# Optimization experiments

Hardware: AMD Instinct MI355X
Metric: run time of the kernel (lower is better)

Reference implementation:

```python
import jax, jax.numpy as jnp
import numpy as np

B, N, E = 4, 10000, 80000
DN, DE, DG = 64, 16, 32
D, H, L = 256, 8, 3
DH = D // H


def _ln(x, s, b, eps=1e-6):
    m = x.mean(-1, keepdims=True)
    v = ((x - m) ** 2).mean(-1, keepdims=True)
    return (x - m) * jax.lax.rsqrt(v + eps) * s + b


def setup_inputs() -> dict:
    key = jax.random.key(0)
    ks = jax.random.split(key, 20)
    sc = 0.02
    p = {}
    # graph data
    p['node_features'] = jax.random.normal(ks[0], (B, N, DN), jnp.float32)
    p['edge_features'] = jax.random.normal(ks[1], (B, E, DE), jnp.float32)
    p['global_features'] = jax.random.normal(ks[2], (B, 1, DG), jnp.float32)
    p['edge_list'] = jax.random.randint(ks[3], (B, E, 2), 0, N)
    p['edge_mask'] = jax.random.bernoulli(ks[4], 0.9, (B, E))
    p['node_mask'] = jax.random.bernoulli(ks[5], 0.95, (B, N))
    p['current_agent_node_ind'] = jax.random.randint(ks[6], (B,), 0, N)
    # input projections
    p['W_node_in'] = jax.random.normal(ks[7], (DN + DG, D)) * sc
    p['b_node_in'] = jnp.zeros((D,))
    p['W_edge_in'] = jax.random.normal(ks[8], (DE, D)) * sc
    p['b_edge_in'] = jnp.zeros((D,))
    p['ln_edge_s'] = jnp.ones((D,)); p['ln_edge_b'] = jnp.zeros((D,))
    # stacked GCN layers: message Dense over concat([h_sender, edge_feat])
    p['gcn_W'] = jax.random.normal(ks[9], (L, 2 * D, D)) * sc
    p['gcn_b'] = jnp.zeros((L, D))
    p['ln_s'] = jnp.ones((L, D)); p['ln_b'] = jnp.zeros((L, D))
    # PGAT params
    p['lnq_s'] = jnp.ones((D,)); p['lnq_b'] = jnp.zeros((D,))
    p['lnk_s'] = jnp.ones((D,)); p['lnk_b'] = jnp.zeros((D,))
    p['Wq'] = jax.random.normal(ks[10], (D, D)) * sc; p['bq'] = jnp.zeros((D,))
    p['Wk'] = jax.random.normal(ks[11], (D, D)) * sc; p['bk'] = jnp.zeros((D,))
    p['Wv'] = jax.random.normal(ks[12], (D, D)) * sc; p['bv'] = jnp.zeros((D,))
    p['Wo'] = jax.random.normal(ks[13], (D, D)) * sc; p['bo'] = jnp.zeros((D,))
    p['lnf_s'] = jnp.ones((D,)); p['lnf_b'] = jnp.zeros((D,))
    return p


def reference(node_features, edge_features, global_features, edge_list, edge_mask,
              node_mask, current_agent_node_ind,
              W_node_in, b_node_in, W_edge_in, b_edge_in, ln_edge_s, ln_edge_b,
              gcn_W, gcn_b, ln_s, ln_b,
              lnq_s, lnq_b, lnk_s, lnk_b, Wq, bq, Wk, bk, Wv, bv, Wo, bo,
              lnf_s, lnf_b):
    senders = edge_list[..., 0]
    receivers = edge_list[..., 1]
    # masked-edge handling: original sets indices to -1 so scatter drops them;
    # we mask explicitly (same math) with safe indices.
    s_safe = jnp.where(edge_mask, senders, 0)
    r_safe = jnp.where(edge_mask, receivers, 0)
    emf = edge_mask.astype(node_features.dtype)  # [B, E]

    gf = jnp.broadcast_to(global_features, node_features.shape[:-1] + (DG,))
    h = jnp.concatenate([node_features, gf], axis=-1) @ W_node_in + b_node_in  # [B,N,D]
    e = jax.nn.relu(_ln(edge_features @ W_edge_in + b_edge_in, ln_edge_s, ln_edge_b))  # [B,E,D]

    seg = jax.vmap(lambda m, r: jax.ops.segment_sum(m, r, num_segments=N))
    deg = jnp.maximum(seg(emf[..., None], r_safe), 1.0)  # [B,N,1]

    for i in range(L):
        hn = jax.nn.relu(_ln(h, ln_s[i], ln_b[i]))
        hs = jnp.take_along_axis(hn, s_safe[..., None], axis=-2)  # [B,E,D] gather
        msg = jnp.concatenate([hs, e], axis=-1) @ gcn_W[i] + gcn_b[i]
        msg = msg * emf[..., None]
        agg = seg(msg, r_safe) / deg  # normalized (mean) aggregation
        h = hn + agg  # residual

    # agent node gather: [B,1,D]
    q_in = jnp.take_along_axis(h, current_agent_node_ind[:, None, None], axis=-2)

    # PGAT: masked multi-head attention of agent query over all nodes
    q = _ln(q_in, lnq_s, lnq_b)
    k = _ln(h, lnk_s, lnk_b)
    Q = (q @ Wq + bq).reshape(B, 1, H, DH)
    K = (k @ Wk + bk).reshape(B, N, H, DH)
    V = (k @ Wv + bv).reshape(B, N, H, DH)
    scores = jnp.einsum('bqhd,bkhd->bhqk', Q, K) / jnp.asarray(np.sqrt(DH), Q.dtype)
    scores = jnp.where(node_mask[:, None, None, :], scores, -1e9)
    attn = jax.nn.softmax(scores, axis=-1)
    o = jnp.einsum('bhqk,bkhd->bqhd', attn, V).reshape(B, 1, D)
    x = q_in + (o @ Wo + bo)  # residual
    x = jax.nn.relu(_ln(x, lnf_s, lnf_b))
    return x.reshape(B, D)  # rearrange '... n d -> ... (n d)' with n=1
```

## Files before the change

kernel.cpp:

```cpp
#include <hip/hip_runtime.h>
#include <hip/hip_bf16.h>

#define B_ 4
#define N_ 10000
#define E_ 80000
#define D_ 256
#define BN_ (B_*N_)
#define MPAD 40064

typedef __attribute__((ext_vector_type(8))) short short8;
typedef __attribute__((ext_vector_type(4))) float f32x4;
typedef __attribute__((ext_vector_type(4))) unsigned short u16x4;

static __device__ __forceinline__ float wave_sum(float v){
  #pragma unroll
  for(int o=32;o>0;o>>=1) v += __shfl_xor(v, o);
  return v;
}

static __device__ __forceinline__ float block_sum(float v, float* red){
  v = wave_sum(v);
  int w = threadIdx.x >> 6;
  if((threadIdx.x & 63) == 0) red[w] = v;
  __syncthreads();
  float r = (red[0] + red[1]) + (red[2] + red[3]);
  __syncthreads();
  return r;
}

static __device__ __forceinline__ unsigned short f2bf(float f){
  unsigned u = __float_as_uint(f);
  return (unsigned short)((u + 0x7fffu + ((u>>16)&1u)) >> 16);
}
static __device__ __forceinline__ float bf2f(unsigned short b){
  return __uint_as_float(((unsigned)b) << 16);
}

__global__ __launch_bounds__(256) void k_node_in(
    const float* __restrict__ nf, const float* __restrict__ gf,
    const float* __restrict__ W, const float* __restrict__ bias,
    const float* __restrict__ lns, const float* __restrict__ lnb,
    unsigned short* __restrict__ hnbf){
  __shared__ float in_s[16][96];
  __shared__ float h_s[16][256];
  int base = blockIdx.x * 16;
  int tid = threadIdx.x;
  for(int idx = tid; idx < 16*96; idx += 256){
    int i = idx / 96, k = idx - i*96;
    int row = base + i;
    int b = row / N_;
    float v = (k < 64) ? nf[(size_t)row*64 + k] : gf[b*32 + (k-64)];
    in_s[i][k] = v;
  }
  __syncthreads();
  int c = tid;
  float acc[16];
  #pragma unroll
  for(int i=0;i<16;i++) acc[i]=0.f;
  for(int k=0;k<96;k+=4){
    float w0 = W[(k+0)*D_+c], w1 = W[(k+1)*D_+c];
    float w2 = W[(k+2)*D_+c], w3 = W[(k+3)*D_+c];
    #pragma unroll
    for(int i=0;i<16;i++){
      float4 a = *reinterpret_cast<const float4*>(&in_s[i][k]);
      acc[i] += a.x*w0 + a.y*w1 + a.z*w2 + a.w*w3;
    }
  }
  float bc = bias[c];
  #pragma unroll
  for(int i=0;i<16;i++) h_s[i][c] = acc[i] + bc;
  __syncthreads();
  int wv = tid>>6, lane = tid&63;
  float4 s4 = *reinterpret_cast<const float4*>(&lns[lane*4]);
  float4 b4 = *reinterpret_cast<const float4*>(&lnb[lane*4]);
  #pragma unroll
  for(int rr=0; rr<4; ++rr){
    int i = wv*4 + rr;
    float4 x = *reinterpret_cast<const float4*>(&h_s[i][lane*4]);
    float sum = x.x+x.y+x.z+x.w;
    float sq = x.x*x.x+x.y*x.y+x.z*x.z+x.w*x.w;
    #pragma unroll
    for(int o=32;o>0;o>>=1){ sum += __shfl_xor(sum,o); sq += __shfl_xor(sq,o); }
    float mean = sum*(1.f/256.f);
    float var = sq*(1.f/256.f) - mean*mean;
    float rs = rsqrtf(var + 1e-6f);
    u16x4 o;
    o.x = f2bf(fmaxf((x.x-mean)*rs*s4.x + b4.x, 0.f));
    o.y = f2bf(fmaxf((x.y-mean)*rs*s4.y + b4.y, 0.f));
    o.z = f2bf(fmaxf((x.z-mean)*rs*s4.z + b4.z, 0.f));
    o.w = f2bf(fmaxf((x.w-mean)*rs*s4.w + b4.w, 0.f));
    *reinterpret_cast<u16x4*>(&hnbf[(size_t)(base+i)*D_ + lane*4]) = o;
  }
}

__global__ __launch_bounds__(256) void k_hist(
    const int* __restrict__ el, const int* __restrict__ emask,
    int* __restrict__ counts){
  int e = blockIdx.x*256 + threadIdx.x;
  if(e >= B_*E_) return;
  if(emask[e]){
    int b = e / E_;
    int r = el[(size_t)e*2 + 1];
    atomicAdd(&counts[b*N_ + r], 1);
  }
}

__global__ __launch_bounds__(1024) void k_scan(
    const int* __restrict__ counts, int* __restrict__ offsets){
  __shared__ int wsum[16];
  int tid = threadIdx.x;
  int base = tid*40;
  int s = 0;
  #pragma unroll
  for(int i=0;i<40;i++){ int idx=base+i; s += (idx<BN_)?counts[idx]:0; }
  int lane = tid&63, w = tid>>6;
  int incl = s;
  #pragma unroll
  for(int o=1;o<64;o<<=1){ int v=__shfl_up(incl,o); if(lane>=o) incl+=v; }
  if(lane==63) wsum[w]=incl;
  __syncthreads();
  if(tid<16){
    int v = wsum[tid];
    #pragma unroll
    for(int o=1;o<16;o<<=1){ int u=__shfl_up(v,o); if(tid>=o) v+=u; }
    wsum[tid]=v;
  }
  __syncthreads();
  int run = ((w>0)?wsum[w-1]:0) + incl - s;
  #pragma unroll
  for(int i=0;i<40;i++){
    int idx=base+i;
    if(idx<BN_){ offsets[idx]=run; run += counts[idx]; }
  }
  if(tid==1023) offsets[BN_]=run;
}

__global__ __launch_bounds__(256) void k_eprep(
    const float* __restrict__ W, const float* __restrict__ be,
    float* __restrict__ prep){
  int t = threadIdx.x;
  int i = t >> 4, j = t & 15;
  float m = 0.f;
  for(int c=0;c<256;c++) m += W[i*256+c]*W[j*256+c];
  prep[t] = m;
  if(t < 16){
    float v=0.f, wb=0.f;
    for(int c=0;c<256;c++){ v += W[t*256+c]*be[c]; wb += W[t*256+c]; }
    prep[256+t] = v;
    prep[272+t] = wb*(1.f/256.f);
  }
  if(t == 0){
    float bb=0.f, ss=0.f;
    for(int c=0;c<256;c++){ bb += be[c]; ss += be[c]*be[c]; }
    prep[288] = bb*(1.f/256.f);
    prep[289] = ss;
  }
}

__global__ __launch_bounds__(256) void k_fill(
    const int* __restrict__ el, const int* __restrict__ emask,
    const float* __restrict__ ef, const float* __restrict__ prep,
    const int* __restrict__ offsets, int* __restrict__ cursor,
    int* __restrict__ s_send, float* __restrict__ ef_slot,
    float* __restrict__ stats){
  __shared__ float M_s[290];
  for(int i=threadIdx.x; i<290; i+=256) M_s[i] = prep[i];
  __syncthreads();
  int e = blockIdx.x*256 + threadIdx.x;
  if(e >= B_*E_) return;
  if(!emask[e]) return;
  int b = e / E_;
  int s = el[(size_t)e*2], r = el[(size_t)e*2 + 1];
  int bn = b*N_ + r;
  int pos = offsets[bn] + atomicAdd(&cursor[bn], 1);
  s_send[pos] = b*N_ + s;
  const float4* src = reinterpret_cast<const float4*>(ef + (size_t)e*16);
  float4 f0=src[0], f1=src[1], f2=src[2], f3=src[3];
  float4* dst = reinterpret_cast<float4*>(ef_slot + (size_t)pos*16);
  dst[0]=f0; dst[1]=f1; dst[2]=f2; dst[3]=f3;
  float f[16] = {f0.x,f0.y,f0.z,f0.w, f1.x,f1.y,f1.z,f1.w,
                 f2.x,f2.y,f2.z,f2.w, f3.x,f3.y,f3.z,f3.w};
  float mean = M_s[288];
  #pragma unroll
  for(int k=0;k<16;k++) mean += f[k]*M_s[272+k];
  float q = M_s[289];
  #pragma unroll
  for(int i=0;i<16;i++){
    float pi = 2.f*M_s[256+i];
    #pragma unroll
    for(int j=0;j<16;j++) pi += M_s[i*16+j]*f[j];
    q += f[i]*pi;
  }
  float var = q*(1.f/256.f) - mean*mean;
  float rstd = rsqrtf(var + 1e-6f);
  stats[(size_t)pos*2]   = mean;
  stats[(size_t)pos*2+1] = rstd;
}

__global__ __launch_bounds__(256) void k_wt(
    const float* __restrict__ gcnW, unsigned short* __restrict__ Wt){
  __shared__ float sm[32][33];
  int bid = blockIdx.x;
  int l = bid >> 7;
  int t = bid & 127;
  int k0 = (t >> 3)*32, n0 = (t & 7)*32;
  int r = threadIdx.x >> 3;
  int c4 = (threadIdx.x & 7)*4;
  const float* src = gcnW + (size_t)l*512*256;
  float4 v = *reinterpret_cast<const float4*>(&src[(size_t)(k0+r)*256 + n0 + c4]);
  sm[r][c4+0]=v.x; sm[r][c4+1]=v.y; sm[r][c4+2]=v.z; sm[r][c4+3]=v.w;
  __syncthreads();
  u16x4 o;
  o.x = f2bf(sm[c4+0][r]); o.y = f2bf(sm[c4+1][r]);
  o.z = f2bf(sm[c4+2][r]); o.w = f2bf(sm[c4+3][r]);
  *reinterpret_cast<u16x4*>(&Wt[(size_t)l*256*512 + (size_t)(n0+r)*512 + k0 + c4]) = o;
}

#define PROJ(F0,F1,F2,F3,COMP) (be4.COMP \
  + F0.x*w[0].COMP + F0.y*w[1].COMP + F0.z*w[2].COMP + F0.w*w[3].COMP \
  + F1.x*w[4].COMP + F1.y*w[5].COMP + F1.z*w[6].COMP + F1.w*w[7].COMP \
  + F2.x*w[8].COMP + F2.y*w[9].COMP + F2.z*w[10].COMP + F2.w*w[11].COMP \
  + F3.x*w[12].COMP + F3.y*w[13].COMP + F3.z*w[14].COMP + F3.w*w[15].COMP)

__global__ __launch_bounds__(256) void k_se_wave(
    const float* __restrict__ ef_slot, const float* __restrict__ stats,
    const float* __restrict__ W, const float* __restrict__ be,
    const float* __restrict__ lns, const float* __restrict__ lnb,
    const int* __restrict__ offsets, unsigned short* __restrict__ Abf){
  int bn = blockIdx.x*4 + (threadIdx.x>>6);
  int lane = threadIdx.x & 63;
  int c = lane*4;
  float4 w[16];
  #pragma unroll
  for(int k=0;k<16;k++) w[k] = *reinterpret_cast<const float4*>(&W[k*D_ + c]);
  float4 be4 = *reinterpret_cast<const float4*>(&be[c]);
  float4 s4  = *reinterpret_cast<const float4*>(&lns[c]);
  float4 b4  = *reinterpret_cast<const float4*>(&lnb[c]);
  int beg = __builtin_amdgcn_readfirstlane(offsets[bn]);
  int end = __builtin_amdgcn_readfirstlane(offsets[bn+1]);
  float a0=0.f,a1=0.f,a2=0.f,a3=0.f;
  int slot = beg;
  for(; slot+2 <= end; slot += 2){
    const float4* e0 = reinterpret_cast<const float4*>(ef_slot + (size_t)slot*16);
    const float4* e1 = reinterpret_cast<const float4*>(ef_slot + (size_t)(slot+1)*16);
    float2 st0 = *reinterpret_cast<const float2*>(stats + (size_t)slot*2);
    float2 st1 = *reinterpret_cast<const float2*>(stats + (size_t)(slot+1)*2);
    float4 f0=e0[0], f1=e0[1], f2=e0[2], f3=e0[3];
    float4 g0=e1[0], g1=e1[1], g2=e1[2], g3=e1[3];
    float t0=PROJ(f0,f1,f2,f3,x), t1=PROJ(f0,f1,f2,f3,y);
    float t2=PROJ(f0,f1,f2,f3,z), t3=PROJ(f0,f1,f2,f3,w);
    float u0=PROJ(g0,g1,g2,g3,x), u1=PROJ(g0,g1,g2,g3,y);
    float u2=PROJ(g0,g1,g2,g3,z), u3=PROJ(g0,g1,g2,g3,w);
    float m0=st0.x, r0=st0.y, m1=st1.x, r1=st1.y;
    a0 += fmaxf((t0-m0)*r0*s4.x + b4.x, 0.f) + fmaxf((u0-m1)*r1*s4.x + b4.x, 0.f);
    a1 += fmaxf((t1-m0)*r0*s4.y + b4.y, 0.f) + fmaxf((u1-m1)*r1*s4.y + b4.y, 0.f);
    a2 += fmaxf((t2-m0)*r0*s4.z + b4.z, 0.f) + fmaxf((u2-m1)*r1*s4.z + b4.z, 0.f);
    a3 += fmaxf((t3-m0)*r0*s4.w + b4.w, 0.f) + fmaxf((u3-m1)*r1*s4.w + b4.w, 0.f);
  }
  if(slot < end){
    const float4* e0 = reinterpret_cast<const float4*>(ef_slot + (size_t)slot*16);
    float2 st0 = *reinterpret_cast<const float2*>(stats + (size_t)slot*2);
    float4 f0=e0[0], f1=e0[1], f2=e0[2], f3=e0[3];
    float t0=PROJ(f0,f1,f2,f3,x), t1=PROJ(f0,f1,f2,f3,y);
    float t2=PROJ(f0,f1,f2,f3,z), t3=PROJ(f0,f1,f2,f3,w);
    float m0=st0.x, r0=st0.y;
    a0 += fmaxf((t0-m0)*r0*s4.x + b4.x, 0.f);
    a1 += fmaxf((t1-m0)*r0*s4.y + b4.y, 0.f);
    a2 += fmaxf((t2-m0)*r0*s4.z + b4.z, 0.f);
    a3 += fmaxf((t3-m0)*r0*s4.w + b4.w, 0.f);
  }
  u16x4 o; o.x=f2bf(a0); o.y=f2bf(a1); o.z=f2bf(a2); o.w=f2bf(a3);
  *reinterpret_cast<u16x4*>(Abf + (size_t)bn*512 + 256 + c) = o;
}

__global__ __launch_bounds__(256) void k_ln_relu(
    const float* __restrict__ h, const float* __restrict__ s,
    const float* __restrict__ b, unsigned short* __restrict__ hnbf){
  int row = blockIdx.x*4 + (threadIdx.x>>6);
  int lane = threadIdx.x & 63;
  int c = lane*4;
  float4 x = *reinterpret_cast<const float4*>(&h[(size_t)row*D_ + c]);
  float sum = x.x+x.y+x.z+x.w;
  float sq = x.x*x.x+x.y*x.y+x.z*x.z+x.w*x.w;
  #pragma unroll
  for(int o=32;o>0;o>>=1){ sum += __shfl_xor(sum,o); sq += __shfl_xor(sq,o); }
  float mean = sum*(1.f/256.f);
  float var = sq*(1.f/256.f) - mean*mean;
  float rs = rsqrtf(var + 1e-6f);
  float4 s4 = *reinterpret_cast<const float4*>(&s[c]);
  float4 b4 = *reinterpret_cast<const float4*>(&b[c]);
  u16x4 o;
  o.x = f2bf(fmaxf((x.x-mean)*rs*s4.x + b4.x, 0.f));
  o.y = f2bf(fmaxf((x.y-mean)*rs*s4.y + b4.y, 0.f));
  o.z = f2bf(fmaxf((x.z-mean)*rs*s4.z + b4.z, 0.f));
  o.w = f2bf(fmaxf((x.w-mean)*rs*s4.w + b4.w, 0.f));
  *reinterpret_cast<u16x4*>(&hnbf[(size_t)row*D_ + c]) = o;
}

__global__ __launch_bounds__(256) void k_agg(
    const unsigned short* __restrict__ hnbf, const int* __restrict__ offsets,
    const int* __restrict__ s_send, unsigned short* __restrict__ Abf){
  int bn = blockIdx.x*4 + (threadIdx.x>>6);
  int lane = threadIdx.x & 63;
  int beg = __builtin_amdgcn_readfirstlane(offsets[bn]);
  int end = __builtin_amdgcn_readfirstlane(offsets[bn+1]);
  float a0=0.f,a1=0.f,a2=0.f,a3=0.f;
  int slot = beg;
  for(; slot+4 <= end; slot += 4){
    int sr0 = s_send[slot],   sr1 = s_send[slot+1];
    int sr2 = s_send[slot+2], sr3 = s_send[slot+3];
    u16x4 v0 = *reinterpret_cast<const u16x4*>(hnbf + (size_t)sr0*D_ + lane*4);
    u16x4 v1 = *reinterpret_cast<const u16x4*>(hnbf + (size_t)sr1*D_ + lane*4);
    u16x4 v2 = *reinterpret_cast<const u16x4*>(hnbf + (size_t)sr2*D_ + lane*4);
    u16x4 v3 = *reinterpret_cast<const u16x4*>(hnbf + (size_t)sr3*D_ + lane*4);
    a0 += bf2f(v0.x)+bf2f(v1.x)+bf2f(v2.x)+bf2f(v3.x);
    a1 += bf2f(v0.y)+bf2f(v1.y)+bf2f(v2.y)+bf2f(v3.y);
    a2 += bf2f(v0.z)+bf2f(v1.z)+bf2f(v2.z)+bf2f(v3.z);
    a3 += bf2f(v0.w)+bf2f(v1.w)+bf2f(v2.w)+bf2f(v3.w);
  }
  for(; slot < end; ++slot){
    int sr = s_send[slot];
    u16x4 v = *reinterpret_cast<const u16x4*>(hnbf + (size_t)sr*D_ + lane*4);
    a0 += bf2f(v.x); a1 += bf2f(v.y); a2 += bf2f(v.z); a3 += bf2f(v.w);
  }
  u16x4 o; o.x=f2bf(a0); o.y=f2bf(a1); o.z=f2bf(a2); o.w=f2bf(a3);
  *reinterpret_cast<u16x4*>(Abf + (size_t)bn*512 + lane*4) = o;
}

__global__ __launch_bounds__(256) void k_gemm_mfma(
    const unsigned short* __restrict__ Abf,
    const unsigned short* __restrict__ Wt,
    const float* __restrict__ bias,
    const int* __restrict__ counts,
    const unsigned short* __restrict__ hnbf,
    float* __restrict__ hout){
  __shared__ unsigned short A_s[128*32];
  __shared__ unsigned short B_s[128*32];
  int bid = blockIdx.x;
  int row0 = (bid>>1)*128;
  int col0 = (bid&1)*128;
  int tid = threadIdx.x;
  int lane = tid & 63;
  int wid = tid >> 6;
  int wr = wid >> 1, wc = wid & 1;
  f32x4 acc[4][4];
  #pragma unroll
  for(int m=0;m<4;m++)
    #pragma unroll
    for(int n=0;n<4;n++) acc[m][n] = (f32x4){0.f,0.f,0.f,0.f};

  int sr = tid >> 1;
  int sc0 = (tid & 1)*2;
  const unsigned short* agp = Abf + (size_t)(row0+sr)*512;
  const unsigned short* bgp = Wt  + (size_t)(col0+sr)*512;
  unsigned swA0 = (unsigned)(sr*64 + (((sc0  ) ^ (sr&3))*16));
  unsigned swA1 = (unsigned)(sr*64 + (((sc0+1) ^ (sr&3))*16));
  int frow = lane & 15;
  int fsw = (lane >> 4) ^ (lane & 3);

  for(int k0=0; k0<512; k0+=32){
    short8 a0 = *reinterpret_cast<const short8*>(agp + k0 + sc0*8);
    short8 a1 = *reinterpret_cast<const short8*>(agp + k0 + sc0*8 + 8);
    short8 b0 = *reinterpret_cast<const short8*>(bgp + k0 + sc0*8);
    short8 b1 = *reinterpret_cast<const short8*>(bgp + k0 + sc0*8 + 8);
    __syncthreads();
    *reinterpret_cast<short8*>((char*)A_s + swA0) = a0;
    *reinterpret_cast<short8*>((char*)A_s + swA1) = a1;
    *reinterpret_cast<short8*>((char*)B_s + swA0) = b0;
    *reinterpret_cast<short8*>((char*)B_s + swA1) = b1;
    __syncthreads();
    short8 af[4], bfr[4];
    #pragma unroll
    for(int m=0;m<4;m++){
      int r = wr*64 + m*16 + frow;
      af[m] = *reinterpret_cast<const short8*>((const char*)A_s + r*64 + fsw*16);
    }
    #pragma unroll
    for(int n=0;n<4;n++){
      int r = wc*64 + n*16 + frow;
      bfr[n] = *reinterpret_cast<const short8*>((const char*)B_s + r*64 + fsw*16);
    }
    #pragma unroll
    for(int m=0;m<4;m++)
      #pragma unroll
      for(int n=0;n<4;n++)
        acc[m][n] = __builtin_amdgcn_mfma_f32_16x16x32_bf16(af[m], bfr[n], acc[m][n], 0, 0, 0);
  }
  #pragma unroll
  for(int m=0;m<4;m++){
    #pragma unroll
    for(int n=0;n<4;n++){
      int col = col0 + wc*64 + n*16 + (lane&15);
      int rbase = row0 + wr*64 + m*16 + (lane>>4)*4;
      float bcol = bias[col];
      #pragma unroll
      for(int j=0;j<4;j++){
        int r = rbase + j;
        if(r < BN_){
          float cnt = (float)counts[r];
          float inv = 1.f / fmaxf(cnt, 1.f);
          hout[(size_t)r*D_ + col] = bf2f(hnbf[(size_t)r*D_ + col]) + (acc[m][n][j] + cnt*bcol)*inv;
        }
      }
    }
  }
}

__global__ __launch_bounds__(256) void k_qprep(
    const float* __restrict__ h, const int* __restrict__ agent,
    const float* __restrict__ lnq_s, const float* __restrict__ lnq_b,
    const float* __restrict__ Wq, const float* __restrict__ bq,
    const float* __restrict__ Wk, const float* __restrict__ bk,
    float* __restrict__ q_in, float* __restrict__ Wq_eff,
    float* __restrict__ qconst){
  __shared__ float q_s[256];
  __shared__ float Q_s[256];
  __shared__ float red[4];
  int b = blockIdx.x, c = threadIdx.x;
  size_t row = (size_t)(b*N_ + agent[b]);
  float x = h[row*D_ + c];
  q_in[b*D_ + c] = x;
  float s1 = block_sum(x, red);
  float mean = s1*(1.f/256.f);
  float d = x - mean;
  float s2 = block_sum(d*d, red);
  float q = d * rsqrtf(s2*(1.f/256.f) + 1e-6f) * lnq_s[c] + lnq_b[c];
  q_s[c] = q;
  __syncthreads();
  float acc = bq[c];
  for(int k=0;k<256;k++) acc += q_s[k]*Wq[k*D_ + c];
  Q_s[c] = acc;
  __syncthreads();
  const float scale = 0.17677669529663687f;
  for(int idx=c; idx<2048; idx+=256){
    int hh = idx >> 8, dd = idx & 255;
    const float4* wk4 = reinterpret_cast<const float4*>(&Wk[(size_t)dd*D_ + hh*32]);
    const float4* q4  = reinterpret_cast<const float4*>(&Q_s[hh*32]);
    float t = 0.f;
    #pragma unroll
    for(int k4=0;k4<8;k4++){
      float4 w = wk4[k4]; float4 qq = q4[k4];
      t += w.x*qq.x + w.y*qq.y + w.z*qq.z + w.w*qq.w;
    }
    Wq_eff[b*2048 + hh*256 + dd] = t*scale;
  }
  if(c < 8){
    float t = 0.f;
    for(int dh=0; dh<32; dh++) t += Q_s[c*32+dh]*bk[c*32+dh];
    qconst[b*8 + c] = t*scale;
  }
}

__global__ __launch_bounds__(256) void k_scores(
    const float* __restrict__ h, const float* __restrict__ lnk_s,
    const float* __restrict__ lnk_b, const float* __restrict__ Wq_eff,
    const float* __restrict__ qconst, const int* __restrict__ nmask,
    unsigned short* __restrict__ kbuf, float* __restrict__ scores){
  __shared__ float wq_s[2048];
  int row0 = blockIdx.x * 4;
  int b = row0 / N_;
  for(int i=threadIdx.x; i<2048; i+=256) wq_s[i] = Wq_eff[b*2048 + i];
  __syncthreads();
  int wave = threadIdx.x >> 6, lane = threadIdx.x & 63;
  int row = row0 + wave;
  int n = row - b*N_;
  int c = lane*4;
  float4 x = *reinterpret_cast<const float4*>(&h[(size_t)row*D_ + c]);
  float sum = x.x+x.y+x.z+x.w;
  float sq = x.x*x.x+x.y*x.y+x.z*x.z+x.w*x.w;
  #pragma unroll
  for(int o=32;o>0;o>>=1){ sum += __shfl_xor(sum,o); sq += __shfl_xor(sq,o); }
  float mean = sum*(1.f/256.f);
  float var = sq*(1.f/256.f) - mean*mean;
  float rs = rsqrtf(var + 1e-6f);
  float4 s4 = *reinterpret_cast<const float4*>(&lnk_s[c]);
  float4 b4 = *reinterpret_cast<const float4*>(&lnk_b[c]);
  float4 kv;
  kv.x = (x.x-mean)*rs*s4.x + b4.x;
  kv.y = (x.y-mean)*rs*s4.y + b4.y;
  kv.z = (x.z-mean)*rs*s4.z + b4.z;
  kv.w = (x.w-mean)*rs*s4.w + b4.w;
  u16x4 kb; kb.x=f2bf(kv.x); kb.y=f2bf(kv.y); kb.z=f2bf(kv.z); kb.w=f2bf(kv.w);
  *reinterpret_cast<u16x4*>(&kbuf[(size_t)row*D_ + c]) = kb;
  bool valid = nmask[row] != 0;
  #pragma unroll
  for(int hh=0; hh<8; hh++){
    float4 w = *reinterpret_cast<const float4*>(&wq_s[hh*256 + c]);
    float p = kv.x*w.x + kv.y*w.y + kv.z*w.z + kv.w*w.w;
    p = wave_sum(p);
    if(lane==0) scores[(size_t)(b*8+hh)*N_ + n] = valid ? (p + qconst[b*8+hh]) : -1e9f;
  }
}

__global__ __launch_bounds__(256) void k_softA(
    const float* __restrict__ scores, float* __restrict__ pm,
    float* __restrict__ ps){
  __shared__ float red[4];
  int bh = blockIdx.x / 10;
  int c0 = (blockIdx.x % 10) * 1000;
  int tid = threadIdx.x;
  float m = -3e38f;
  for(int n=tid; n<1000; n+=256) m = fmaxf(m, scores[(size_t)bh*N_ + c0 + n]);
  #pragma unroll
  for(int o=32;o>0;o>>=1) m = fmaxf(m, __shfl_xor(m,o));
  if((tid&63)==0) red[tid>>6] = m;
  __syncthreads();
  m = fmaxf(fmaxf(red[0],red[1]), fmaxf(red[2],red[3]));
  __syncthreads();
  float s = 0.f;
  for(int n=tid; n<1000; n+=256) s += __expf(scores[(size_t)bh*N_ + c0 + n] - m);
  s = block_sum(s, red);
  if(tid==0){ pm[blockIdx.x] = m; ps[blockIdx.x] = s; }
}

__global__ __launch_bounds__(64) void k_softB(
    const float* __restrict__ pm, const float* __restrict__ ps,
    float* __restrict__ mg, float* __restrict__ inv){
  int t = threadIdx.x;
  if(t < 32){
    float m = -3e38f;
    #pragma unroll
    for(int c=0;c<10;c++) m = fmaxf(m, pm[t*10+c]);
    float s = 0.f;
    #pragma unroll
    for(int c=0;c<10;c++) s += ps[t*10+c]*__expf(pm[t*10+c]-m);
    mg[t] = m;
    inv[t] = 1.f/s;
  }
}

__global__ __launch_bounds__(256) void k_kbar(
    const unsigned short* __restrict__ kbuf, const float* __restrict__ scores,
    const float* __restrict__ mg, const float* __restrict__ inv,
    float* __restrict__ kbar){
  __shared__ float p_s[8][40];
  int b = blockIdx.x / 250;
  int n0 = (blockIdx.x % 250) * 40;
  for(int i=threadIdx.x; i<8*40; i+=256){
    int hh = i/40, nn = i - hh*40;
    p_s[hh][nn] = __expf(scores[(size_t)(b*8+hh)*N_ + n0 + nn] - mg[b*8+hh]);
  }
  __syncthreads();
  int c = threadIdx.x;
  float acc[8] = {0.f,0.f,0.f,0.f,0.f,0.f,0.f,0.f};
  for(int nn=0; nn<40; ++nn){
    float kv = bf2f(kbuf[(size_t)(b*N_ + n0 + nn)*D_ + c]);
    #pragma unroll
    for(int hh=0;hh<8;hh++) acc[hh] += p_s[hh][nn]*kv;
  }
  #pragma unroll
  for(int hh=0;hh<8;hh++)
    atomicAdd(&kbar[(b*8+hh)*D_ + c], acc[hh]*inv[b*8+hh]);
}

__global__ __launch_bounds__(256) void k_final(
    const float* __restrict__ kbar, const float* __restrict__ Wv,
    const float* __restrict__ bv, const float* __restrict__ Wo,
    const float* __restrict__ bo, const float* __restrict__ q_in,
    const float* __restrict__ lnf_s, const float* __restrict__ lnf_b,
    float* __restrict__ out){
  __shared__ float kb_s[2048];
  __shared__ float o_s[256];
  __shared__ float red[4];
  int b = blockIdx.x, c = threadIdx.x;
  for(int i=c; i<2048; i+=256) kb_s[i] = kbar[b*2048 + i];
  __syncthreads();
  int hh = c >> 5;
  float o = bv[c];
  for(int d=0; d<256; d++) o += kb_s[hh*256 + d]*Wv[(size_t)d*D_ + c];
  o_s[c] = o;
  __syncthreads();
  float y = bo[c] + q_in[b*D_ + c];
  for(int d=0; d<256; d++) y += o_s[d]*Wo[(size_t)d*D_ + c];
  float s1 = block_sum(y, red);
  float mean = s1*(1.f/256.f);
  float dd = y - mean;
  float s2 = block_sum(dd*dd, red);
  float v = dd * rsqrtf(s2*(1.f/256.f) + 1e-6f) * lnf_s[c] + lnf_b[c];
  out[b*D_ + c] = fmaxf(v, 0.f);
}

extern "C" void kernel_launch(void* const* d_in, const int* in_sizes, int n_in,
                              void* d_out, int out_size, void* d_ws, size_t ws_size,
                              hipStream_t stream){
  const float* nf    = (const float*)d_in[0];
  const float* ef    = (const float*)d_in[1];
  const float* gf    = (const float*)d_in[2];
  const int*   el    = (const int*)d_in[3];
  const int*   emask = (const int*)d_in[4];
  const int*   nmask = (const int*)d_in[5];
  const int*   agent = (const int*)d_in[6];
  const float* W_node = (const float*)d_in[7];
  const float* b_node = (const float*)d_in[8];
  const float* W_edge = (const float*)d_in[9];
  const float* b_edge = (const float*)d_in[10];
  const float* ln_e_s = (const float*)d_in[11];
  const float* ln_e_b = (const float*)d_in[12];
  const float* gcn_W  = (const float*)d_in[13];
  const float* gcn_b  = (const float*)d_in[14];
  const float* ln_s   = (const float*)d_in[15];
  const float* ln_b   = (const float*)d_in[16];
  const float* lnq_s  = (const float*)d_in[17];
  const float* lnq_b  = (const float*)d_in[18];
  const float* lnk_s  = (const float*)d_in[19];
  const float* lnk_b  = (const float*)d_in[20];
  const float* Wq = (const float*)d_in[21];
  const float* bq = (const float*)d_in[22];
  const float* Wv = (const float*)d_in[25];
  const float* bv = (const float*)d_in[26];
  const float* Wk = (const float*)d_in[23];
  const float* bk = (const float*)d_in[24];
  const float* Wo = (const float*)d_in[27];
  const float* bo = (const float*)d_in[28];
  const float* lnf_s = (const float*)d_in[29];
  const float* lnf_b = (const float*)d_in[30];
  float* out = (float*)d_out;

  const size_t ND = (size_t)BN_*D_;
  char* w = (char*)d_ws;
  float* h_buf = (float*)w;                   w += ND*4;
  unsigned short* hn_bf = (unsigned short*)w; w += (size_t)MPAD*D_*2;
  unsigned short* A_bf = (unsigned short*)w;  w += (size_t)MPAD*512*2;
  unsigned short* Wt = (unsigned short*)w;    w += (size_t)3*256*512*2;
  float* scores = (float*)w;                  w += (size_t)B_*8*N_*4;
  float* q_in = (float*)w;                    w += B_*D_*4;
  float* Wq_eff = (float*)w;                  w += B_*8*D_*4;
  float* qconst = (float*)w;                  w += B_*8*4;
  float* pm = (float*)w;                      w += 320*4;
  float* ps = (float*)w;                      w += 320*4;
  float* mg = (float*)w;                      w += 32*4;
  float* invs = (float*)w;                    w += 32*4;
  float* kbar = (float*)w;                    w += B_*8*D_*4;
  float* prep = (float*)w;                    w += 512*4;
  int* counts = (int*)w;                      w += BN_*4;
  int* cursor = (int*)w;                      w += BN_*4;
  int* offsets = (int*)w;                     w += (BN_+1)*4;
  int* s_send = (int*)w;                      w += (size_t)B_*E_*4;
  float* ef_slot = (float*)w;                 w += (size_t)B_*E_*16*4;
  float* stats = (float*)w;                   w += (size_t)B_*E_*2*4;
  unsigned short* kbuf = (unsigned short*)A_bf;

  hipMemsetAsync(counts, 0, sizeof(int)*(size_t)2*BN_, stream);
  hipMemsetAsync(kbar, 0, sizeof(float)*(size_t)B_*8*D_, stream);

  k_node_in<<<BN_/16, 256, 0, stream>>>(nf, gf, W_node, b_node, ln_s, ln_b, hn_bf);
  k_hist<<<B_*E_/256, 256, 0, stream>>>(el, emask, counts);
  k_scan<<<1, 1024, 0, stream>>>(counts, offsets);
  k_eprep<<<1, 256, 0, stream>>>(W_edge, b_edge, prep);
  k_fill<<<B_*E_/256, 256, 0, stream>>>(el, emask, ef, prep, offsets, cursor,
                                        s_send, ef_slot, stats);
  k_wt<<<384, 256, 0, stream>>>(gcn_W, Wt);
  k_se_wave<<<BN_/4, 256, 0, stream>>>(ef_slot, stats, W_edge, b_edge,
                                       ln_e_s, ln_e_b, offsets, A_bf);

  for(int i=0;i<3;i++){
    k_agg<<<BN_/4, 256, 0, stream>>>(hn_bf, offsets, s_send, A_bf);
    k_gemm_mfma<<<(MPAD/128)*2, 256, 0, stream>>>(A_bf, Wt + (size_t)i*256*512,
                                                  gcn_b + i*D_, counts, hn_bf, h_buf);
    if(i < 2)
      k_ln_relu<<<BN_/4, 256, 0, stream>>>(h_buf, ln_s + (i+1)*D_, ln_b + (i+1)*D_, hn_bf);
  }

  k_qprep<<<B_, 256, 0, stream>>>(h_buf, agent, lnq_s, lnq_b, Wq, bq, Wk, bk,
                                  q_in, Wq_eff, qconst);
  k_scores<<<BN_/4, 256, 0, stream>>>(h_buf, lnk_s, lnk_b, Wq_eff, qconst, nmask,
                                      kbuf, scores);
  k_softA<<<320, 256, 0, stream>>>(scores, pm, ps);
  k_softB<<<1, 64, 0, stream>>>(pm, ps, mg, invs);
  k_kbar<<<B_*250, 256, 0, stream>>>(kbuf, scores, mg, invs, kbar);
  k_final<<<B_, 256, 0, stream>>>(kbar, Wv, bv, Wo, bo, q_in, lnf_s, lnf_b, out);
}
```

Measured before the change: 546.1 us.

## Replace single-block prefix scan with three-pass multi-block scan

The exclusive scan over 40000 per-node edge counts was done by one 1024-thread block, each thread serially walking 40 elements with strided uncoalesced loads. It is now split into a per-block reduce, a single-block scan of the 157 block sums, and a per-block local scan that adds the block offset. This spreads the work across many CUs with coalesced access, at the cost of two extra kernel launches and small extra workspace buffers.

Result: faster. 481.1 us (-11.9%).

```diff
diff --git a/kernel.cpp b/kernel.cpp
--- a/kernel.cpp
+++ b/kernel.cpp
@@ -7,6 +7,7 @@
 #define D_ 256
 #define BN_ (B_*N_)
 #define MPAD 40064
+#define SCAN_NBLK ((BN_ + 255) / 256)
 
 typedef __attribute__((ext_vector_type(8))) short short8;
 typedef __attribute__((ext_vector_type(4))) float f32x4;
@@ -105,34 +106,53 @@
   }
 }
 
-__global__ __launch_bounds__(1024) void k_scan(
-    const int* __restrict__ counts, int* __restrict__ offsets){
-  __shared__ int wsum[16];
-  int tid = threadIdx.x;
-  int base = tid*40;
-  int s = 0;
-  #pragma unroll
-  for(int i=0;i<40;i++){ int idx=base+i; s += (idx<BN_)?counts[idx]:0; }
-  int lane = tid&63, w = tid>>6;
-  int incl = s;
+__global__ __launch_bounds__(256) void k_scanA(
+    const int* __restrict__ counts, int* __restrict__ bsum){
+  __shared__ int red[4];
+  int idx = blockIdx.x*256 + threadIdx.x;
+  int x = (idx < BN_) ? counts[idx] : 0;
+  int lane = threadIdx.x & 63, w = threadIdx.x >> 6;
+  int s = x;
+  #pragma unroll
+  for(int o=32;o>0;o>>=1) s += __shfl_xor(s, o);
+  if(lane == 0) red[w] = s;
+  __syncthreads();
+  if(threadIdx.x == 0) bsum[blockIdx.x] = red[0]+red[1]+red[2]+red[3];
+}
+
+__global__ __launch_bounds__(256) void k_scanB(
+    const int* __restrict__ bsum, int* __restrict__ boff){
+  __shared__ int ws[4];
+  int t = threadIdx.x;
+  int x = (t < SCAN_NBLK) ? bsum[t] : 0;
+  int lane = t & 63, w = t >> 6;
+  int incl = x;
   #pragma unroll
   for(int o=1;o<64;o<<=1){ int v=__shfl_up(incl,o); if(lane>=o) incl+=v; }
-  if(lane==63) wsum[w]=incl;
-  __syncthreads();
-  if(tid<16){
-    int v = wsum[tid];
-    #pragma unroll
-    for(int o=1;o<16;o<<=1){ int u=__shfl_up(v,o); if(tid>=o) v+=u; }
-    wsum[tid]=v;
-  }
-  __syncthreads();
-  int run = ((w>0)?wsum[w-1]:0) + incl - s;
-  #pragma unroll
-  for(int i=0;i<40;i++){
-    int idx=base+i;
-    if(idx<BN_){ offsets[idx]=run; run += counts[idx]; }
-  }
-  if(tid==1023) offsets[BN_]=run;
+  if(lane == 63) ws[w] = incl;
+  __syncthreads();
+  int pre = 0;
+  for(int i=0;i<w;i++) pre += ws[i];
+  if(t < SCAN_NBLK) boff[t] = pre + incl - x;
+}
+
+__global__ __launch_bounds__(256) void k_scanC(
+    const int* __restrict__ counts, const int* __restrict__ boff,
+    int* __restrict__ offsets){
+  __shared__ int ws[4];
+  int idx = blockIdx.x*256 + threadIdx.x;
+  int x = (idx < BN_) ? counts[idx] : 0;
+  int lane = threadIdx.x & 63, w = threadIdx.x >> 6;
+  int incl = x;
+  #pragma unroll
+  for(int o=1;o<64;o<<=1){ int v=__shfl_up(incl,o); if(lane>=o) incl+=v; }
+  if(lane == 63) ws[w] = incl;
+  __syncthreads();
+  int pre = boff[blockIdx.x];
+  for(int i=0;i<w;i++) pre += ws[i];
+  int excl = pre + incl - x;
+  if(idx < BN_) offsets[idx] = excl;
+  if(idx == BN_-1) offsets[BN_] = excl + x;
 }
 
 __global__ __launch_bounds__(256) void k_eprep(
@@ -606,10 +626,10 @@
   const float* lnk_b  = (const float*)d_in[20];
   const float* Wq = (const float*)d_in[21];
   const float* bq = (const float*)d_in[22];
+  const float* Wk = (const float*)d_in[23];
+  const float* bk = (const float*)d_in[24];
   const float* Wv = (const float*)d_in[25];
   const float* bv = (const float*)d_in[26];
-  const float* Wk = (const float*)d_in[23];
-  const float* bk = (const float*)d_in[24];
   const float* Wo = (const float*)d_in[27];
   const float* bo = (const float*)d_in[28];
   const float* lnf_s = (const float*)d_in[29];
@@ -635,6 +655,8 @@
   int* counts = (int*)w;                      w += BN_*4;
   int* cursor = (int*)w;                      w += BN_*4;
   int* offsets = (int*)w;                     w += (BN_+1)*4;
+  int* bsum = (int*)w;                        w += SCAN_NBLK*4;
+  int* boff = (int*)w;                        w += SCAN_NBLK*4;
   int* s_send = (int*)w;                      w += (size_t)B_*E_*4;
   float* ef_slot = (float*)w;                 w += (size_t)B_*E_*16*4;
   float* stats = (float*)w;                   w += (size_t)B_*E_*2*4;
@@ -645,7 +667,9 @@
 
   k_node_in<<<BN_/16, 256, 0, stream>>>(nf, gf, W_node, b_node, ln_s, ln_b, hn_bf);
   k_hist<<<B_*E_/256, 256, 0, stream>>>(el, emask, counts);
-  k_scan<<<1, 1024, 0, stream>>>(counts, offsets);
+  k_scanA<<<SCAN_NBLK, 256, 0, stream>>>(counts, bsum);
+  k_scanB<<<1, 256, 0, stream>>>(bsum, boff);
+  k_scanC<<<SCAN_NBLK, 256, 0, stream>>>(counts, boff, offsets);
   k_eprep<<<1, 256, 0, stream>>>(W_edge, b_edge, prep);
   k_fill<<<B_*E_/256, 256, 0, stream>>>(el, emask, ef, prep, offsets, cursor,
                                         s_send, ef_slot, stats);
```
